# Kernel tuning notes

Measured on AMD Instinct MI355X. Metric: run time of the kernel, lower is better.

Reference implementation:

```python
import jax, jax.numpy as jnp
import numpy as np

B, S, D, H, DH = 2, 2048, 1024, 16, 64
GLOBAL_RATIO = 0.1
LN_EPS = 1e-5


def setup_inputs() -> dict:
    key = jax.random.key(0)
    ks = jax.random.split(key, 8)
    w = lambda k, shape: jax.random.normal(k, shape, jnp.float32) * 0.02
    return {
        'x': jax.random.normal(ks[0], (B, S, D), jnp.float32),
        'Wq': w(ks[1], (D, H * DH)),
        'Wk': w(ks[2], (D, H * DH)),
        'Wv': w(ks[3], (D, H * DH)),
        'Wo': w(ks[4], (H * DH, D)),
        'bo': jnp.zeros((D,), jnp.float32),
        'ln_gamma': jnp.ones((DH,), jnp.float32),
        'ln_beta': jnp.zeros((DH,), jnp.float32),
        'Wg': w(ks[5], (2 * DH, DH)),
        'bg': jnp.zeros((DH,), jnp.float32),
    }


def _layernorm(x, gamma, beta):
    mu = jnp.mean(x, axis=-1, keepdims=True)
    var = jnp.mean(jnp.square(x - mu), axis=-1, keepdims=True)
    return (x - mu) * jax.lax.rsqrt(var + LN_EPS) * gamma + beta


def reference(x, Wq, Wk, Wv, Wo, bo, ln_gamma, ln_beta, Wg, bg):
    b, s, _ = x.shape
    # projections -> [b, h, n, d]
    split = lambda t: t.reshape(b, s, H, DH).transpose(0, 2, 1, 3)
    q = split(x @ Wq)
    k = split(x @ Wk)
    v = split(x @ Wv)
    scale = DH ** -0.5

    # local (full) attention: manual QK^T / softmax / AV
    scores = jnp.einsum('bhnd,bhmd->bhnm', q, k) * scale  # [b,h,s,s]
    attn = jax.nn.softmax(scores, axis=-1)
    local_out = jnp.einsum('bhnm,bhmd->bhnd', attn, v)

    # cross-segment fusion: top-k keys by norm per (b, h)
    num_global = max(1, int(s * GLOBAL_RATIO))
    key_norms = jnp.linalg.norm(k, axis=-1)  # [b,h,s]
    _, top_idx = jax.lax.top_k(key_norms, num_global)  # [b,h,g]
    idx = top_idx[..., None]  # [b,h,g,1]
    global_k = jnp.take_along_axis(k, idx, axis=2)  # [b,h,g,d]
    global_v = jnp.take_along_axis(v, idx, axis=2)
    g_scores = jnp.einsum('bhnd,bhgd->bhng', q, global_k) * scale
    g_attn = jax.nn.softmax(g_scores, axis=-1)
    global_out = jnp.einsum('bhng,bhgd->bhnd', g_attn, global_v)
    global_out = _layernorm(global_out, ln_gamma, ln_beta)

    # learned gate over [local, global]
    cat = jnp.concatenate([local_out, global_out], axis=-1)  # [b,h,s,2d]
    gate = jax.nn.sigmoid(cat @ Wg + bg)
    fused = gate * local_out + (1.0 - gate) * global_out

    out = fused.transpose(0, 2, 1, 3).reshape(b, s, H * DH)  # b h n d -> b n (h d)
    return out @ Wo + bo
```

## Files before the change

### kernel.cpp

```cpp
#include <hip/hip_runtime.h>


constexpr int SEQ    = 2048;
constexpr int DMODEL = 1024;
constexpr int NH     = 16;
constexpr int DHEAD  = 64;
constexpr int BHT    = 32;
constexpr int NG     = 204;
constexpr int NGPAD  = 256;
constexpr float LNEPS = 1e-5f;

typedef __attribute__((ext_vector_type(8))) short short8;
typedef __attribute__((ext_vector_type(4))) short short4v;
typedef __attribute__((ext_vector_type(4))) float f32x4;

__device__ __forceinline__ unsigned short f2bf(float f) {
    unsigned int u = __float_as_uint(f);
    u += 0x7FFFu + ((u >> 16) & 1u);
    return (unsigned short)(u >> 16);
}
__device__ __forceinline__ float bf2f(unsigned short b) {
    return __uint_as_float(((unsigned int)b) << 16);
}

__global__ __launch_bounds__(256)
void prep_k(const float* __restrict__ x,
            const float* __restrict__ Wq, const float* __restrict__ Wv,
            const float* __restrict__ Wo, const float* __restrict__ Wk,
            const float* __restrict__ Wg,
            unsigned short* __restrict__ xh, unsigned short* __restrict__ xl,
            unsigned short* __restrict__ Wqt, unsigned short* __restrict__ Wvt,
            unsigned short* __restrict__ Wot, unsigned short* __restrict__ Wkh,
            unsigned short* __restrict__ Wkl, unsigned short* __restrict__ Wgt)
{
    const int bid = blockIdx.x;
    const int tid = threadIdx.x;

    if (bid < 2048) {
        int i = (bid * 256 + tid) << 3;
        short8 h, l;
#pragma unroll
        for (int j = 0; j < 8; ++j) {
            float v = x[i + j];
            unsigned short hb = f2bf(v);
            h[j] = (short)hb;
            l[j] = (short)f2bf(v - bf2f(hb));
        }
        *(short8*)(xh + i) = h;
        *(short8*)(xl + i) = l;
        return;
    }
    if (bid == 3072) {
#pragma unroll
        for (int i = 0; i < 32; ++i) {
            int o = tid * 32 + i;
            int dg = o >> 7, jj = o & 127;
            Wgt[o] = f2bf(Wg[jj * 64 + dg]);
        }
        return;
    }

    __shared__ float tile[64][68];
    const int sub = bid - 2048;
    const int which = sub >> 8;
    const int b = sub & 255;
    const int n0 = (b & 15) * 64, k0 = (b >> 4) * 64;
    const float* W = (which == 0) ? Wq : (which == 1) ? Wv : (which == 2) ? Wo : Wk;
    const int Kd = DMODEL, Nd = DMODEL;

#pragma unroll
    for (int p = 0; p < 4; ++p) {
        int c = tid + (p << 8);
        int r = c >> 4, c4 = (c & 15) << 2;
        *(float4*)&tile[r][c4] = *(const float4*)(W + (size_t)(k0 + r) * Nd + n0 + c4);
    }
    __syncthreads();
#pragma unroll
    for (int p = 0; p < 4; ++p) {
        int c = tid + (p << 8);
        int n = c >> 4, k4 = (c & 15) << 2;
        if (which < 3) {
            unsigned short* Wt = (which == 0) ? Wqt : (which == 1) ? Wvt : Wot;
            short4v o;
#pragma unroll
            for (int j = 0; j < 4; ++j) o[j] = (short)f2bf(tile[k4 + j][n]);
            *(short4v*)(Wt + (size_t)(n0 + n) * Kd + k0 + k4) = o;
        } else {
            short4v oh, ol;
#pragma unroll
            for (int j = 0; j < 4; ++j) {
                float v = tile[k4 + j][n];
                unsigned short hb = f2bf(v);
                oh[j] = (short)hb;
                ol[j] = (short)f2bf(v - bf2f(hb));
            }
            *(short4v*)(Wkh + (size_t)(n0 + n) * Kd + k0 + k4) = oh;
            *(short4v*)(Wkl + (size_t)(n0 + n) * Kd + k0 + k4) = ol;
        }
    }
}

__global__ __launch_bounds__(512)
void gemm_bf16_k(const unsigned short* __restrict__ A,
                 const unsigned short* __restrict__ Bt,
                 const float* __restrict__ bias,
                 void* __restrict__ outv, void* __restrict__ outv2,
                 unsigned short* __restrict__ vtout,
                 int M, int N, int K, int mode)
{
    __shared__ __align__(16) unsigned short As[128][72];
    __shared__ __align__(16) unsigned short Bs[128][72];
    const int tid = threadIdx.x;
    const int lane = tid & 63, wave = tid >> 6;
    const int quad = lane >> 4, ln = lane & 15;
    const int mh = (wave >> 2) << 6;
    const int nh = (wave & 3) << 5;
    const int m0 = blockIdx.y * 128, n0 = blockIdx.x * 128;

    f32x4 acc[4][2];
#pragma unroll
    for (int i = 0; i < 4; ++i)
#pragma unroll
        for (int j = 0; j < 2; ++j) acc[i][j] = (f32x4){0.f, 0.f, 0.f, 0.f};

    short8 areg[2], breg[2];
#pragma unroll
    for (int p = 0; p < 2; ++p) {
        int c = tid + (p << 9);
        int row = c >> 3, col8 = (c & 7) << 3;
        areg[p] = *(const short8*)(A + (size_t)(m0 + row) * K + col8);
        breg[p] = *(const short8*)(Bt + (size_t)(n0 + row) * K + col8);
    }

    for (int k0 = 0; k0 < K; k0 += 64) {
        __syncthreads();
#pragma unroll
        for (int p = 0; p < 2; ++p) {
            int c = tid + (p << 9);
            int row = c >> 3, col8 = (c & 7) << 3;
            *(short8*)&As[row][col8] = areg[p];
            *(short8*)&Bs[row][col8] = breg[p];
        }
        __syncthreads();
        if (k0 + 64 < K) {
#pragma unroll
            for (int p = 0; p < 2; ++p) {
                int c = tid + (p << 9);
                int row = c >> 3, col8 = (c & 7) << 3;
                areg[p] = *(const short8*)(A + (size_t)(m0 + row) * K + k0 + 64 + col8);
                breg[p] = *(const short8*)(Bt + (size_t)(n0 + row) * K + k0 + 64 + col8);
            }
        }
#pragma unroll
        for (int ch = 0; ch < 2; ++ch) {
            short8 af[4], bf[2];
#pragma unroll
            for (int mt = 0; mt < 4; ++mt)
                af[mt] = *(const short8*)&As[mh + mt * 16 + ln][ch * 32 + quad * 8];
#pragma unroll
            for (int nt = 0; nt < 2; ++nt)
                bf[nt] = *(const short8*)&Bs[nh + nt * 16 + ln][ch * 32 + quad * 8];
#pragma unroll
            for (int mt = 0; mt < 4; ++mt)
#pragma unroll
                for (int nt = 0; nt < 2; ++nt)
                    acc[mt][nt] = __builtin_amdgcn_mfma_f32_16x16x32_bf16(
                        af[mt], bf[nt], acc[mt][nt], 0, 0, 0);
        }
    }

    if (mode == 0) {
        float* out = (float*)outv;
#pragma unroll
        for (int mt = 0; mt < 4; ++mt)
#pragma unroll
            for (int nt = 0; nt < 2; ++nt)
#pragma unroll
                for (int r = 0; r < 4; ++r) {
                    int m = m0 + mh + mt * 16 + quad * 4 + r;
                    int n = n0 + nh + nt * 16 + ln;
                    out[(size_t)m * N + n] = acc[mt][nt][r] + bias[n];
                }
    } else {
#pragma unroll
        for (int mt = 0; mt < 4; ++mt)
#pragma unroll
            for (int nt = 0; nt < 2; ++nt) {
                int n = n0 + nh + nt * 16 + ln;
                int mb = m0 + mh + mt * 16 + quad * 4;
                int b = mb >> 11, s0 = mb & (SEQ - 1);
                int d = n & 63;
                if (n < DMODEL) {
                    int h = n >> 6;
                    unsigned short* qp_ =
                        (unsigned short*)outv + ((size_t)(b * NH + h) * SEQ + s0) * DHEAD + d;
#pragma unroll
                    for (int r = 0; r < 4; ++r)
                        qp_[(size_t)r * DHEAD] = f2bf(acc[mt][nt][r] * 0.125f);
                } else {
                    int h = (n >> 6) - NH;
                    unsigned short* vp_ =
                        (unsigned short*)outv2 + ((size_t)(b * NH + h) * SEQ + s0) * DHEAD + d;
                    short4v tv;
#pragma unroll
                    for (int r = 0; r < 4; ++r) {
                        unsigned short bv = f2bf(acc[mt][nt][r]);
                        vp_[(size_t)r * DHEAD] = bv;
                        tv[r] = (short)bv;
                    }
                    *(short4v*)(vtout + ((size_t)(b * NH + h) * DHEAD + d) * SEQ + s0) = tv;
                }
            }
    }
}

__global__ __launch_bounds__(512)
void gemm_kproj_mfma(const unsigned short* __restrict__ xh,
                     const unsigned short* __restrict__ xl,
                     const unsigned short* __restrict__ Wh,
                     const unsigned short* __restrict__ Wl,
                     unsigned short* __restrict__ kout,
                     float* __restrict__ norms2)
{
    __shared__ __align__(16) unsigned short Ah[64][72];
    __shared__ __align__(16) unsigned short Al[64][72];
    __shared__ __align__(16) unsigned short Bh[128][72];
    __shared__ __align__(16) unsigned short Bl[128][72];
    const int K = DMODEL;
    const int tid = threadIdx.x;
    const int lane = tid & 63, wave = tid >> 6;
    const int quad = lane >> 4, ln = lane & 15;
    const int mh = (wave >> 1) << 4;
    const int nh = (wave & 1) << 6;
    const int m0 = blockIdx.y * 64, n0 = blockIdx.x * 128;

    f32x4 acc[4];
#pragma unroll
    for (int j = 0; j < 4; ++j) acc[j] = (f32x4){0.f, 0.f, 0.f, 0.f};

    const int arow = tid >> 3, acol8 = (tid & 7) << 3;
    short8 ahreg, alreg, bhreg[2], blreg[2];
    {
        size_t ga = (size_t)(m0 + arow) * K + acol8;
        ahreg = *(const short8*)(xh + ga);
        alreg = *(const short8*)(xl + ga);
#pragma unroll
        for (int p = 0; p < 2; ++p) {
            int c = tid + (p << 9);
            int row = c >> 3, col8 = (c & 7) << 3;
            size_t gb = (size_t)(n0 + row) * K + col8;
            bhreg[p] = *(const short8*)(Wh + gb);
            blreg[p] = *(const short8*)(Wl + gb);
        }
    }

    for (int k0 = 0; k0 < K; k0 += 64) {
        __syncthreads();
        *(short8*)&Ah[arow][acol8] = ahreg;
        *(short8*)&Al[arow][acol8] = alreg;
#pragma unroll
        for (int p = 0; p < 2; ++p) {
            int c = tid + (p << 9);
            int row = c >> 3, col8 = (c & 7) << 3;
            *(short8*)&Bh[row][col8] = bhreg[p];
            *(short8*)&Bl[row][col8] = blreg[p];
        }
        __syncthreads();
        if (k0 + 64 < K) {
            size_t ga = (size_t)(m0 + arow) * K + k0 + 64 + acol8;
            ahreg = *(const short8*)(xh + ga);
            alreg = *(const short8*)(xl + ga);
#pragma unroll
            for (int p = 0; p < 2; ++p) {
                int c = tid + (p << 9);
                int row = c >> 3, col8 = (c & 7) << 3;
                size_t gb = (size_t)(n0 + row) * K + k0 + 64 + col8;
                bhreg[p] = *(const short8*)(Wh + gb);
                blreg[p] = *(const short8*)(Wl + gb);
            }
        }
#pragma unroll
        for (int ch = 0; ch < 2; ++ch) {
            short8 bh4[4], bl4[4];
#pragma unroll
            for (int nt = 0; nt < 4; ++nt) {
                bh4[nt] = *(const short8*)&Bh[nh + nt * 16 + ln][ch * 32 + quad * 8];
                bl4[nt] = *(const short8*)&Bl[nh + nt * 16 + ln][ch * 32 + quad * 8];
            }
            short8 ah = *(const short8*)&Ah[mh + ln][ch * 32 + quad * 8];
            short8 al = *(const short8*)&Al[mh + ln][ch * 32 + quad * 8];
#pragma unroll
            for (int nt = 0; nt < 4; ++nt) {
                acc[nt] = __builtin_amdgcn_mfma_f32_16x16x32_bf16(ah, bh4[nt], acc[nt], 0, 0, 0);
                acc[nt] = __builtin_amdgcn_mfma_f32_16x16x32_bf16(ah, bl4[nt], acc[nt], 0, 0, 0);
                acc[nt] = __builtin_amdgcn_mfma_f32_16x16x32_bf16(al, bh4[nt], acc[nt], 0, 0, 0);
            }
        }
    }

    const int h = (n0 + nh) >> 6;
#pragma unroll
    for (int r = 0; r < 4; ++r) {
        int m = m0 + mh + quad * 4 + r;
        int b = m >> 11, s = m & (SEQ - 1);
        size_t rowbase = ((size_t)(b * NH + h) * SEQ + s) * DHEAD;
#pragma unroll
        for (int nt = 0; nt < 4; ++nt)
            kout[rowbase + nt * 16 + ln] = f2bf(acc[nt][r]);
        float s2 = acc[0][r] * acc[0][r] + acc[1][r] * acc[1][r] +
                   acc[2][r] * acc[2][r] + acc[3][r] * acc[3][r];
#pragma unroll
        for (int off = 1; off <= 8; off <<= 1)
            s2 += __shfl_xor(s2, off);
        if (ln == 0)
            norms2[(size_t)(b * NH + h) * SEQ + s] = s2;
    }
}

__global__ __launch_bounds__(512)
void topk_gather_k(const float* __restrict__ norms2,
                   const unsigned short* __restrict__ k,
                   const unsigned short* __restrict__ v,
                   unsigned short* __restrict__ gk,
                   unsigned short* __restrict__ gvt)
{
    __shared__ unsigned long long keys[SEQ];
    __shared__ int tix[NGPAD];
    __shared__ __align__(16) unsigned short T[64][72];
    const int bh = blockIdx.x;
    const int tid = threadIdx.x;
    const float* nb = norms2 + (size_t)bh * SEQ;
    const size_t base = (size_t)bh * SEQ * DHEAD;

    for (int i = tid; i < SEQ; i += 512) {
        float nrm = sqrtf(nb[i]);
        keys[i] = ((unsigned long long)__float_as_uint(nrm) << 32) |
                  (unsigned int)(0xFFFFFFFFu - (unsigned int)i);
    }
    __syncthreads();
    for (int kk = 2; kk <= SEQ; kk <<= 1) {
        for (int j = kk >> 1; j > 0; j >>= 1) {
            for (int i = tid; i < SEQ; i += 512) {
                int ixj = i ^ j;
                if (ixj > i) {
                    unsigned long long a = keys[i], b = keys[ixj];
                    bool up = ((i & kk) == 0);
                    if ((a > b) == up) { keys[i] = b; keys[ixj] = a; }
                }
            }
            __syncthreads();
        }
    }
    if (tid < NGPAD) {
        tix[tid] = (tid < NG)
            ? (int)(0xFFFFFFFFu - (unsigned int)(keys[SEQ - 1 - tid] & 0xFFFFFFFFu))
            : 0;
    }
    __syncthreads();

    for (int t = 0; t < NGPAD / 64; ++t) {
        {
            int idx = tid;
            int row = idx >> 3, col8 = (idx & 7) << 3;
            int g = t * 64 + row;
            short8 kv = (short8)0, vv = (short8)0;
            if (g < NG) {
                int sidx = tix[g];
                kv = *(const short8*)(k + base + (size_t)sidx * DHEAD + col8);
                vv = *(const short8*)(v + base + (size_t)sidx * DHEAD + col8);
            }
            *(short8*)(gk + ((size_t)bh * NGPAD + g) * DHEAD + col8) = kv;
            *(short8*)&T[row][col8] = vv;
        }
        __syncthreads();
        {
            int idx = tid;
            int d = idx >> 3, k8 = (idx & 7) << 3;
            short8 o;
#pragma unroll
            for (int i = 0; i < 8; ++i) o[i] = (short)T[k8 + i][d];
            *(short8*)(gvt + ((size_t)bh * DHEAD + d) * NGPAD + t * 64 + k8) = o;
        }
        __syncthreads();
    }
}

__global__ __launch_bounds__(256, 2)
void attn_fused_k(const unsigned short* __restrict__ qb,
                  const unsigned short* __restrict__ kb,
                  const unsigned short* __restrict__ vt,
                  const unsigned short* __restrict__ gk,
                  const unsigned short* __restrict__ gvt,
                  const unsigned short* __restrict__ Wgt,
                  const float* __restrict__ gamma,
                  const float* __restrict__ beta,
                  const float* __restrict__ bg,
                  unsigned short* __restrict__ fused)
{
    __shared__ __align__(16) unsigned short Ks[64][72];
    __shared__ __align__(16) unsigned short Vt[64][72];
    __shared__ __align__(16) unsigned short Ps[128][72];
    __shared__ __align__(16) unsigned short Wgs[64][136];
    const int flat = blockIdx.x;
    const int bh = ((flat >> 7) << 3) | (flat & 7);
    const int q0 = ((flat >> 3) & 15) * 128;
    const int tid = threadIdx.x;
    const int lane = tid & 63, wave = tid >> 6;
    const int quad = lane >> 4, ln = lane & 15;
    const size_t base = (size_t)bh * SEQ * DHEAD;
    const unsigned short* gkb = gk + (size_t)bh * NGPAD * DHEAD;
    const unsigned short* gvb = gvt + (size_t)bh * DHEAD * NGPAD;

#pragma unroll
    for (int p = 0; p < 4; ++p) {
        int idx = tid + (p << 8);
        *(short8*)&Wgs[idx >> 4][(idx & 15) << 3] = *(const short8*)(Wgt + idx * 8);
    }

    short8 qf[2][2];
#pragma unroll
    for (int mt = 0; mt < 2; ++mt) {
        const unsigned short* qp = qb + base + (size_t)(q0 + wave * 32 + mt * 16 + ln) * DHEAD;
        qf[mt][0] = *(const short8*)(qp + quad * 8);
        qf[mt][1] = *(const short8*)(qp + 32 + quad * 8);
    }

    f32x4 O[2][4], Og[2][4];
#pragma unroll
    for (int mt = 0; mt < 2; ++mt)
#pragma unroll
        for (int nt = 0; nt < 4; ++nt) {
            O[mt][nt] = (f32x4){0.f, 0.f, 0.f, 0.f};
            Og[mt][nt] = (f32x4){0.f, 0.f, 0.f, 0.f};
        }
    float ls[2][4], lg[2][4];
#pragma unroll
    for (int mt = 0; mt < 2; ++mt)
#pragma unroll
        for (int r = 0; r < 4; ++r) { ls[mt][r] = 0.f; lg[mt][r] = 0.f; }

    short8 kreg[2], vreg[2];
    int srow[2], scol8[2];
#pragma unroll
    for (int p = 0; p < 2; ++p) {
        int idx = tid + (p << 8);
        srow[p] = idx >> 3;
        scol8[p] = (idx & 7) << 3;
        kreg[p] = *(const short8*)(kb + base + (size_t)srow[p] * DHEAD + scol8[p]);
        vreg[p] = *(const short8*)(vt + base + (size_t)srow[p] * SEQ + scol8[p]);
    }

    for (int t = 0; t < SEQ / 64; ++t) {
        __syncthreads();
#pragma unroll
        for (int p = 0; p < 2; ++p) {
            *(short8*)&Ks[srow[p]][scol8[p]] = kreg[p];
            *(short8*)&Vt[srow[p]][scol8[p]] = vreg[p];
        }
        __syncthreads();
        if (t + 1 < SEQ / 64) {
#pragma unroll
            for (int p = 0; p < 2; ++p) {
                kreg[p] = *(const short8*)(kb + base + (size_t)((t + 1) * 64 + srow[p]) * DHEAD + scol8[p]);
                vreg[p] = *(const short8*)(vt + base + (size_t)srow[p] * SEQ + (t + 1) * 64 + scol8[p]);
            }
        } else {
#pragma unroll
            for (int p = 0; p < 2; ++p) {
                kreg[p] = *(const short8*)(gkb + (size_t)srow[p] * DHEAD + scol8[p]);
                vreg[p] = *(const short8*)(gvb + (size_t)srow[p] * NGPAD + scol8[p]);
            }
        }

        f32x4 s[2][4];
#pragma unroll
        for (int mt = 0; mt < 2; ++mt)
#pragma unroll
            for (int nt = 0; nt < 4; ++nt) s[mt][nt] = (f32x4){0.f, 0.f, 0.f, 0.f};
        __builtin_amdgcn_s_setprio(1);
#pragma unroll
        for (int nt = 0; nt < 4; ++nt) {
            short8 kf0 = *(const short8*)&Ks[nt * 16 + ln][quad * 8];
            short8 kf1 = *(const short8*)&Ks[nt * 16 + ln][32 + quad * 8];
#pragma unroll
            for (int mt = 0; mt < 2; ++mt) {
                s[mt][nt] = __builtin_amdgcn_mfma_f32_16x16x32_bf16(qf[mt][0], kf0, s[mt][nt], 0, 0, 0);
                s[mt][nt] = __builtin_amdgcn_mfma_f32_16x16x32_bf16(qf[mt][1], kf1, s[mt][nt], 0, 0, 0);
            }
        }
        __builtin_amdgcn_s_setprio(0);
#pragma unroll
        for (int mt = 0; mt < 2; ++mt)
#pragma unroll
            for (int nt = 0; nt < 4; ++nt)
#pragma unroll
                for (int r = 0; r < 4; ++r) {
                    float p = __expf(s[mt][nt][r]);
                    unsigned int us = __float_as_uint(p) >> 16;
                    Ps[wave * 32 + mt * 16 + quad * 4 + r][nt * 16 + ln] = (unsigned short)us;
                    ls[mt][r] += __uint_as_float(us << 16);
                }
#pragma unroll
        for (int ch = 0; ch < 2; ++ch) {
            short8 pf[2];
#pragma unroll
            for (int mt = 0; mt < 2; ++mt)
                pf[mt] = *(const short8*)&Ps[wave * 32 + mt * 16 + ln][ch * 32 + quad * 8];
            __builtin_amdgcn_s_setprio(1);
#pragma unroll
            for (int nt = 0; nt < 4; ++nt) {
                short8 vf = *(const short8*)&Vt[nt * 16 + ln][ch * 32 + quad * 8];
#pragma unroll
                for (int mt = 0; mt < 2; ++mt)
                    O[mt][nt] = __builtin_amdgcn_mfma_f32_16x16x32_bf16(pf[mt], vf, O[mt][nt], 0, 0, 0);
            }
            __builtin_amdgcn_s_setprio(0);
        }
    }

    for (int t = 0; t < NGPAD / 64; ++t) {
        __syncthreads();
#pragma unroll
        for (int p = 0; p < 2; ++p) {
            *(short8*)&Ks[srow[p]][scol8[p]] = kreg[p];
            *(short8*)&Vt[srow[p]][scol8[p]] = vreg[p];
        }
        __syncthreads();
        if (t + 1 < NGPAD / 64) {
#pragma unroll
            for (int p = 0; p < 2; ++p) {
                kreg[p] = *(const short8*)(gkb + (size_t)((t + 1) * 64 + srow[p]) * DHEAD + scol8[p]);
                vreg[p] = *(const short8*)(gvb + (size_t)srow[p] * NGPAD + (t + 1) * 64 + scol8[p]);
            }
        }

        f32x4 s[2][4];
#pragma unroll
        for (int mt = 0; mt < 2; ++mt)
#pragma unroll
            for (int nt = 0; nt < 4; ++nt) s[mt][nt] = (f32x4){0.f, 0.f, 0.f, 0.f};
        __builtin_amdgcn_s_setprio(1);
#pragma unroll
        for (int nt = 0; nt < 4; ++nt) {
            short8 kf0 = *(const short8*)&Ks[nt * 16 + ln][quad * 8];
            short8 kf1 = *(const short8*)&Ks[nt * 16 + ln][32 + quad * 8];
#pragma unroll
            for (int mt = 0; mt < 2; ++mt) {
                s[mt][nt] = __builtin_amdgcn_mfma_f32_16x16x32_bf16(qf[mt][0], kf0, s[mt][nt], 0, 0, 0);
                s[mt][nt] = __builtin_amdgcn_mfma_f32_16x16x32_bf16(qf[mt][1], kf1, s[mt][nt], 0, 0, 0);
            }
        }
        __builtin_amdgcn_s_setprio(0);
#pragma unroll
        for (int nt = 0; nt < 4; ++nt) {
            bool valid = (t * 64 + nt * 16 + ln) < NG;
#pragma unroll
            for (int mt = 0; mt < 2; ++mt)
#pragma unroll
                for (int r = 0; r < 4; ++r) {
                    float p = valid ? __expf(s[mt][nt][r]) : 0.f;
                    unsigned int us = __float_as_uint(p) >> 16;
                    Ps[wave * 32 + mt * 16 + quad * 4 + r][nt * 16 + ln] = (unsigned short)us;
                    lg[mt][r] += __uint_as_float(us << 16);
                }
        }
#pragma unroll
        for (int ch = 0; ch < 2; ++ch) {
            short8 pf[2];
#pragma unroll
            for (int mt = 0; mt < 2; ++mt)
                pf[mt] = *(const short8*)&Ps[wave * 32 + mt * 16 + ln][ch * 32 + quad * 8];
            __builtin_amdgcn_s_setprio(1);
#pragma unroll
            for (int nt = 0; nt < 4; ++nt) {
                short8 vf = *(const short8*)&Vt[nt * 16 + ln][ch * 32 + quad * 8];
#pragma unroll
                for (int mt = 0; mt < 2; ++mt)
                    Og[mt][nt] = __builtin_amdgcn_mfma_f32_16x16x32_bf16(pf[mt], vf, Og[mt][nt], 0, 0, 0);
            }
            __builtin_amdgcn_s_setprio(0);
        }
    }

#pragma unroll
    for (int off = 1; off <= 8; off <<= 1)
#pragma unroll
        for (int mt = 0; mt < 2; ++mt)
#pragma unroll
            for (int r = 0; r < 4; ++r) {
                ls[mt][r] += __shfl_xor(ls[mt][r], off);
                lg[mt][r] += __shfl_xor(lg[mt][r], off);
            }
    float invl[2][4];
#pragma unroll
    for (int mt = 0; mt < 2; ++mt)
#pragma unroll
        for (int r = 0; r < 4; ++r) invl[mt][r] = 1.f / ls[mt][r];

    float xs[2][4][4];
#pragma unroll
    for (int mt = 0; mt < 2; ++mt)
#pragma unroll
        for (int r = 0; r < 4; ++r) {
            float inv = 1.f / lg[mt][r];
#pragma unroll
            for (int nt = 0; nt < 4; ++nt) xs[mt][nt][r] = Og[mt][nt][r] * inv;
        }
    float mu[2][4], rsd[2][4];
#pragma unroll
    for (int mt = 0; mt < 2; ++mt)
#pragma unroll
        for (int r = 0; r < 4; ++r) {
            float sm = xs[mt][0][r] + xs[mt][1][r] + xs[mt][2][r] + xs[mt][3][r];
#pragma unroll
            for (int off = 1; off <= 8; off <<= 1) sm += __shfl_xor(sm, off);
            mu[mt][r] = sm * (1.f / 64.f);
        }
#pragma unroll
    for (int mt = 0; mt < 2; ++mt)
#pragma unroll
        for (int r = 0; r < 4; ++r) {
            float sv = 0.f;
#pragma unroll
            for (int nt = 0; nt < 4; ++nt) {
                float d = xs[mt][nt][r] - mu[mt][r];
                sv += d * d;
            }
#pragma unroll
            for (int off = 1; off <= 8; off <<= 1) sv += __shfl_xor(sv, off);
            rsd[mt][r] = rsqrtf(sv * (1.f / 64.f) + LNEPS);
        }
#pragma unroll
    for (int nt = 0; nt < 4; ++nt) {
        float g = gamma[nt * 16 + ln], bb = beta[nt * 16 + ln];
#pragma unroll
        for (int mt = 0; mt < 2; ++mt)
#pragma unroll
            for (int r = 0; r < 4; ++r)
                xs[mt][nt][r] = (xs[mt][nt][r] - mu[mt][r]) * rsd[mt][r] * g + bb;
    }

    float lf[2][4][4];
#pragma unroll
    for (int mt = 0; mt < 2; ++mt)
#pragma unroll
        for (int nt = 0; nt < 4; ++nt)
#pragma unroll
            for (int r = 0; r < 4; ++r) {
                lf[mt][nt][r] = O[mt][nt][r] * invl[mt][r];
                Ps[wave * 32 + mt * 16 + quad * 4 + r][nt * 16 + ln] = f2bf(lf[mt][nt][r]);
            }
    f32x4 gacc[2][4];
#pragma unroll
    for (int ng = 0; ng < 4; ++ng) {
        float bgv = bg[ng * 16 + ln];
#pragma unroll
        for (int mt = 0; mt < 2; ++mt)
            gacc[mt][ng] = (f32x4){bgv, bgv, bgv, bgv};
    }
#pragma unroll
    for (int ch = 0; ch < 2; ++ch) {
        short8 af[2];
#pragma unroll
        for (int mt = 0; mt < 2; ++mt)
            af[mt] = *(const short8*)&Ps[wave * 32 + mt * 16 + ln][ch * 32 + quad * 8];
#pragma unroll
        for (int ng = 0; ng < 4; ++ng) {
            short8 bf = *(const short8*)&Wgs[ng * 16 + ln][ch * 32 + quad * 8];
#pragma unroll
            for (int mt = 0; mt < 2; ++mt)
                gacc[mt][ng] = __builtin_amdgcn_mfma_f32_16x16x32_bf16(af[mt], bf, gacc[mt][ng], 0, 0, 0);
        }
    }
#pragma unroll
    for (int mt = 0; mt < 2; ++mt)
#pragma unroll
        for (int nt = 0; nt < 4; ++nt)
#pragma unroll
            for (int r = 0; r < 4; ++r)
                Ps[wave * 32 + mt * 16 + quad * 4 + r][nt * 16 + ln] = f2bf(xs[mt][nt][r]);
#pragma unroll
    for (int ch = 0; ch < 2; ++ch) {
        short8 af[2];
#pragma unroll
        for (int mt = 0; mt < 2; ++mt)
            af[mt] = *(const short8*)&Ps[wave * 32 + mt * 16 + ln][ch * 32 + quad * 8];
#pragma unroll
        for (int ng = 0; ng < 4; ++ng) {
            short8 bf = *(const short8*)&Wgs[ng * 16 + ln][64 + ch * 32 + quad * 8];
#pragma unroll
            for (int mt = 0; mt < 2; ++mt)
                gacc[mt][ng] = __builtin_amdgcn_mfma_f32_16x16x32_bf16(af[mt], bf, gacc[mt][ng], 0, 0, 0);
        }
    }

    const int b = bh >> 4, h = bh & 15;
#pragma unroll
    for (int mt = 0; mt < 2; ++mt)
#pragma unroll
        for (int ng = 0; ng < 4; ++ng)
#pragma unroll
            for (int r = 0; r < 4; ++r) {
                float gt = 1.f / (1.f + __expf(-gacc[mt][ng][r]));
                float f = gt * lf[mt][ng][r] + (1.f - gt) * xs[mt][ng][r];
                int s = q0 + wave * 32 + mt * 16 + quad * 4 + r;
                fused[((size_t)(b * SEQ + s)) * DMODEL + h * DHEAD + ng * 16 + ln] = f2bf(f);
            }
}

extern "C" void kernel_launch(void* const* d_in, const int* in_sizes, int n_in,
                              void* d_out, int out_size, void* d_ws, size_t ws_size,
                              hipStream_t stream)
{
    (void)in_sizes; (void)n_in; (void)out_size; (void)ws_size;
    const float* x    = (const float*)d_in[0];
    const float* Wq   = (const float*)d_in[1];
    const float* Wk   = (const float*)d_in[2];
    const float* Wv   = (const float*)d_in[3];
    const float* Wo   = (const float*)d_in[4];
    const float* bo   = (const float*)d_in[5];
    const float* ln_g = (const float*)d_in[6];
    const float* ln_b = (const float*)d_in[7];
    const float* Wg   = (const float*)d_in[8];
    const float* bg   = (const float*)d_in[9];

    char* w = (char*)d_ws;
    const size_t MB = 1024ull * 1024ull;
    unsigned short* kb16  = (unsigned short*)(w);
    unsigned short* qb16  = (unsigned short*)(w + 8 * MB);
    unsigned short* vb16  = (unsigned short*)(w + 16 * MB);
    unsigned short* vt16  = (unsigned short*)(w + 24 * MB);
    unsigned short* xh    = (unsigned short*)(w + 32 * MB);
    unsigned short* xl    = (unsigned short*)(w + 40 * MB);
    unsigned short* Wqt   = (unsigned short*)(w + 48 * MB);
    unsigned short* Wvt   = (unsigned short*)(w + 50 * MB);
    unsigned short* Wot   = (unsigned short*)(w + 52 * MB);
    unsigned short* Wkh   = (unsigned short*)(w + 54 * MB);
    unsigned short* Wkl   = (unsigned short*)(w + 56 * MB);
    unsigned short* Wgt   = (unsigned short*)(w + 58 * MB);
    float*          norms2= (float*)(w + 59 * MB);
    unsigned short* gk16  = (unsigned short*)(w + 60 * MB);
    unsigned short* gvt16 = (unsigned short*)(w + 61 * MB);
    unsigned short* fusedb = xh;

    const int M = 4096, N = 1024, K = 1024;

    prep_k<<<3073, 256, 0, stream>>>(x, Wq, Wv, Wo, Wk, Wg,
                                     xh, xl, Wqt, Wvt, Wot, Wkh, Wkl, Wgt);

    dim3 gqv(2048 / 128, M / 128);
    gemm_bf16_k<<<gqv, 512, 0, stream>>>(xh, Wqt, nullptr, qb16, vb16, vt16,
                                         M, 2048, K, 3);

    dim3 gkp(N / 128, M / 64);
    gemm_kproj_mfma<<<gkp, 512, 0, stream>>>(xh, xl, Wkh, Wkl, kb16, norms2);

    topk_gather_k<<<BHT, 512, 0, stream>>>(norms2, kb16, vb16, gk16, gvt16);

    attn_fused_k<<<512, 256, 0, stream>>>(qb16, kb16, vt16, gk16, gvt16, Wgt,
                                          ln_g, ln_b, bg, fusedb);

    dim3 go_(N / 128, M / 128);
    gemm_bf16_k<<<go_, 512, 0, stream>>>(fusedb, Wot, bo, (float*)d_out, nullptr,
                                         nullptr, M, N, K, 0);
}
```

Before: 284.4 us.

## Keep softmax probabilities in registers by computing transposed scores for PV MFMA

Swaps the MFMA operands so the score tile comes out transposed (keys along rows). This lets each lane's exponentiated probabilities be fed directly as the A operand of 16x16x16 bf16 MFMAs for the P·V product, without writing P to shared memory and reading it back. Row sums become per-lane partials reduced across quads and then redistributed with shuffles. The cost is twice as many (smaller-K) MFMA instructions for PV and narrower LDS reads of V.

```diff
diff --git a/kernel.cpp b/kernel.cpp
--- a/kernel.cpp
+++ b/kernel.cpp
@@ -433,11 +433,7 @@
             O[mt][nt] = (f32x4){0.f, 0.f, 0.f, 0.f};
             Og[mt][nt] = (f32x4){0.f, 0.f, 0.f, 0.f};
         }
-    float ls[2][4], lg[2][4];
-#pragma unroll
-    for (int mt = 0; mt < 2; ++mt)
-#pragma unroll
-        for (int r = 0; r < 4; ++r) { ls[mt][r] = 0.f; lg[mt][r] = 0.f; }
+    float ls[2] = {0.f, 0.f}, lg[2] = {0.f, 0.f};
 
     short8 kreg[2], vreg[2];
     int srow[2], scol8[2];
@@ -484,38 +480,36 @@
             short8 kf1 = *(const short8*)&Ks[nt * 16 + ln][32 + quad * 8];
 #pragma unroll
             for (int mt = 0; mt < 2; ++mt) {
-                s[mt][nt] = __builtin_amdgcn_mfma_f32_16x16x32_bf16(qf[mt][0], kf0, s[mt][nt], 0, 0, 0);
-                s[mt][nt] = __builtin_amdgcn_mfma_f32_16x16x32_bf16(qf[mt][1], kf1, s[mt][nt], 0, 0, 0);
+                s[mt][nt] = __builtin_amdgcn_mfma_f32_16x16x32_bf16(kf0, qf[mt][0], s[mt][nt], 0, 0, 0);
+                s[mt][nt] = __builtin_amdgcn_mfma_f32_16x16x32_bf16(kf1, qf[mt][1], s[mt][nt], 0, 0, 0);
             }
         }
         __builtin_amdgcn_s_setprio(0);
+
+        short4v pf[2][4];
 #pragma unroll
         for (int mt = 0; mt < 2; ++mt)
 #pragma unroll
             for (int nt = 0; nt < 4; ++nt)
 #pragma unroll
                 for (int r = 0; r < 4; ++r) {
-                    float p = __expf(s[mt][nt][r]);
-                    unsigned int us = __float_as_uint(p) >> 16;
-                    Ps[wave * 32 + mt * 16 + quad * 4 + r][nt * 16 + ln] = (unsigned short)us;
-                    ls[mt][r] += __uint_as_float(us << 16);
+                    unsigned int u = __float_as_uint(__expf(s[mt][nt][r]));
+                    ls[mt] += __uint_as_float(u & 0xFFFF0000u);
+                    pf[mt][nt][r] = (short)(u >> 16);
                 }
-#pragma unroll
-        for (int ch = 0; ch < 2; ++ch) {
-            short8 pf[2];
-#pragma unroll
-            for (int mt = 0; mt < 2; ++mt)
-                pf[mt] = *(const short8*)&Ps[wave * 32 + mt * 16 + ln][ch * 32 + quad * 8];
-            __builtin_amdgcn_s_setprio(1);
-#pragma unroll
-            for (int nt = 0; nt < 4; ++nt) {
-                short8 vf = *(const short8*)&Vt[nt * 16 + ln][ch * 32 + quad * 8];
+
+        __builtin_amdgcn_s_setprio(1);
+#pragma unroll
+        for (int dt = 0; dt < 4; ++dt)
+#pragma unroll
+            for (int ks = 0; ks < 4; ++ks) {
+                short4v vf = *(const short4v*)&Vt[dt * 16 + ln][ks * 16 + quad * 4];
 #pragma unroll
                 for (int mt = 0; mt < 2; ++mt)
-                    O[mt][nt] = __builtin_amdgcn_mfma_f32_16x16x32_bf16(pf[mt], vf, O[mt][nt], 0, 0, 0);
-            }
-            __builtin_amdgcn_s_setprio(0);
-        }
+                    O[mt][dt] = __builtin_amdgcn_mfma_f32_16x16x16bf16_1k(
+                        pf[mt][ks], vf, O[mt][dt], 0, 0, 0);
+            }
+        __builtin_amdgcn_s_setprio(0);
     }
 
     for (int t = 0; t < NGPAD / 64; ++t) {
@@ -546,63 +540,63 @@
             short8 kf1 = *(const short8*)&Ks[nt * 16 + ln][32 + quad * 8];
 #pragma unroll
             for (int mt = 0; mt < 2; ++mt) {
-                s[mt][nt] = __builtin_amdgcn_mfma_f32_16x16x32_bf16(qf[mt][0], kf0, s[mt][nt], 0, 0, 0);
-                s[mt][nt] = __builtin_amdgcn_mfma_f32_16x16x32_bf16(qf[mt][1], kf1, s[mt][nt], 0, 0, 0);
+                s[mt][nt] = __builtin_amdgcn_mfma_f32_16x16x32_bf16(kf0, qf[mt][0], s[mt][nt], 0, 0, 0);
+                s[mt][nt] = __builtin_amdgcn_mfma_f32_16x16x32_bf16(kf1, qf[mt][1], s[mt][nt], 0, 0, 0);
             }
         }
         __builtin_amdgcn_s_setprio(0);
-#pragma unroll
-        for (int nt = 0; nt < 4; ++nt) {
-            bool valid = (t * 64 + nt * 16 + ln) < NG;
-#pragma unroll
-            for (int mt = 0; mt < 2; ++mt)
-#pragma unroll
-                for (int r = 0; r < 4; ++r) {
+
+        short4v pf[2][4];
+#pragma unroll
+        for (int nt = 0; nt < 4; ++nt)
+#pragma unroll
+            for (int r = 0; r < 4; ++r) {
+                bool valid = (t * 64 + nt * 16 + quad * 4 + r) < NG;
+#pragma unroll
+                for (int mt = 0; mt < 2; ++mt) {
                     float p = valid ? __expf(s[mt][nt][r]) : 0.f;
-                    unsigned int us = __float_as_uint(p) >> 16;
-                    Ps[wave * 32 + mt * 16 + quad * 4 + r][nt * 16 + ln] = (unsigned short)us;
-                    lg[mt][r] += __uint_as_float(us << 16);
+                    unsigned int u = __float_as_uint(p);
+                    lg[mt] += __uint_as_float(u & 0xFFFF0000u);
+                    pf[mt][nt][r] = (short)(u >> 16);
                 }
-        }
-#pragma unroll
-        for (int ch = 0; ch < 2; ++ch) {
-            short8 pf[2];
-#pragma unroll
-            for (int mt = 0; mt < 2; ++mt)
-                pf[mt] = *(const short8*)&Ps[wave * 32 + mt * 16 + ln][ch * 32 + quad * 8];
-            __builtin_amdgcn_s_setprio(1);
-#pragma unroll
-            for (int nt = 0; nt < 4; ++nt) {
-                short8 vf = *(const short8*)&Vt[nt * 16 + ln][ch * 32 + quad * 8];
+            }
+
+        __builtin_amdgcn_s_setprio(1);
+#pragma unroll
+        for (int dt = 0; dt < 4; ++dt)
+#pragma unroll
+            for (int ks = 0; ks < 4; ++ks) {
+                short4v vf = *(const short4v*)&Vt[dt * 16 + ln][ks * 16 + quad * 4];
 #pragma unroll
                 for (int mt = 0; mt < 2; ++mt)
-                    Og[mt][nt] = __builtin_amdgcn_mfma_f32_16x16x32_bf16(pf[mt], vf, Og[mt][nt], 0, 0, 0);
-            }
-            __builtin_amdgcn_s_setprio(0);
-        }
-    }
-
-#pragma unroll
-    for (int off = 1; off <= 8; off <<= 1)
-#pragma unroll
-        for (int mt = 0; mt < 2; ++mt)
-#pragma unroll
-            for (int r = 0; r < 4; ++r) {
-                ls[mt][r] += __shfl_xor(ls[mt][r], off);
-                lg[mt][r] += __shfl_xor(lg[mt][r], off);
-            }
-    float invl[2][4];
+                    Og[mt][dt] = __builtin_amdgcn_mfma_f32_16x16x16bf16_1k(
+                        pf[mt][ks], vf, Og[mt][dt], 0, 0, 0);
+            }
+        __builtin_amdgcn_s_setprio(0);
+    }
+
+#pragma unroll
+    for (int mt = 0; mt < 2; ++mt) {
+        ls[mt] += __shfl_xor(ls[mt], 16);
+        ls[mt] += __shfl_xor(ls[mt], 32);
+        lg[mt] += __shfl_xor(lg[mt], 16);
+        lg[mt] += __shfl_xor(lg[mt], 32);
+    }
+    float invl[2][4], invg[2][4];
 #pragma unroll
     for (int mt = 0; mt < 2; ++mt)
 #pragma unroll
-        for (int r = 0; r < 4; ++r) invl[mt][r] = 1.f / ls[mt][r];
+        for (int r = 0; r < 4; ++r) {
+            invl[mt][r] = 1.f / __shfl(ls[mt], quad * 4 + r);
+            invg[mt][r] = 1.f / __shfl(lg[mt], quad * 4 + r);
+        }
 
     float xs[2][4][4];
 #pragma unroll
     for (int mt = 0; mt < 2; ++mt)
 #pragma unroll
         for (int r = 0; r < 4; ++r) {
-            float inv = 1.f / lg[mt][r];
+            float inv = invg[mt][r];
 #pragma unroll
             for (int nt = 0; nt < 4; ++nt) xs[mt][nt][r] = Og[mt][nt][r] * inv;
         }
```

New measurement: 280.2 us. About the same (-1.5%).
